# Performance work log

Measured on AMD Instinct MI355X. Metric: run time of the kernel, lower is better.

Reference implementation:

```python
import jax, jax.numpy as jnp
import numpy as np

NTOKENS = 50257
NHID = 1024
NPC = int(np.ceil(np.sqrt(NTOKENS)))            # 225 tokens per class
NCLASSES = int(np.ceil(NTOKENS / NPC))          # 224 classes
BATCH = 1024
INITRANGE = 0.1


def setup_inputs() -> dict:
    key = jax.random.key(0)
    k1, k2, k3, k4 = jax.random.split(key, 4)
    inputs = jax.random.normal(k1, (BATCH, NHID), dtype=jnp.float32)
    labels = jax.random.randint(k2, (BATCH,), 0, NTOKENS, dtype=jnp.int64)
    layer_top_W = jax.random.uniform(k3, (NHID, NCLASSES), minval=-INITRANGE, maxval=INITRANGE, dtype=jnp.float32)
    layer_top_b = jnp.zeros((NCLASSES,), dtype=jnp.float32)
    layer_bottom_W = jax.random.uniform(k4, (NCLASSES, NHID, NPC), minval=-INITRANGE, maxval=INITRANGE, dtype=jnp.float32)
    layer_bottom_b = jnp.zeros((NCLASSES, NPC), dtype=jnp.float32)
    return {
        "inputs": inputs,
        "labels": labels,
        "layer_top_W": layer_top_W,
        "layer_top_b": layer_top_b,
        "layer_bottom_W": layer_bottom_W,
        "layer_bottom_b": layer_bottom_b,
    }


def reference(inputs, labels, layer_top_W, layer_top_b, layer_bottom_W, layer_bottom_b):
    batch_size = inputs.shape[0]
    # decompose label into (class, within-class) position; old-torch `/` on Long == floor div
    pos_top = labels // NPC            # [B]
    pos_bottom = labels % NPC          # [B]

    # top-level class distribution: [B, nclasses]
    top_logits = inputs @ layer_top_W + layer_top_b
    top_probs = jax.nn.softmax(top_logits, axis=1)

    # gather per-sample class weight slices and do batched matvec:
    # layer_bottom_W[pos_top]: [B, nhid, npc]
    bottom_logits = jnp.einsum("bd,bdc->bc", inputs, layer_bottom_W[pos_top]) + layer_bottom_b[pos_top]
    bottom_probs = jax.nn.softmax(bottom_logits, axis=1)

    rows = jnp.arange(batch_size)
    target_probs = top_probs[rows, pos_top] * bottom_probs[rows, pos_bottom]  # [B]
    return target_probs
```

## Files before the change

### kernel.cpp

```cpp
#include <hip/hip_runtime.h>
#include <math.h>

#define NTOK 50257
#define NHID 1024
#define NPC  225
#define NCLS 224
#define BATCH 1024

#define WS_ORDER_OFS 16
#define WS_ITEMS_OFS 8192
#define WS_PTOP_OFS  16384
#define MAX_ITEMS    352

__global__ __launch_bounds__(256) void k0_group(const int* __restrict__ labels,
                                                int* __restrict__ ws)
{
    __shared__ int cnt[256];
    __shared__ int scan[256];
    __shared__ int iscan[256];
    __shared__ int cur[256];
    const int tid = threadIdx.x;

    cnt[tid] = 0;
    __syncthreads();
    for (int i = tid; i < BATCH; i += 256)
        atomicAdd(&cnt[labels[i] / NPC], 1);
    __syncthreads();

    const int myc = (tid < NCLS) ? cnt[tid] : 0;
    const int myi = (myc + 7) >> 3;
    scan[tid]  = myc;
    iscan[tid] = myi;
    __syncthreads();
    for (int off = 1; off < 256; off <<= 1) {
        int a = (tid >= off) ? scan[tid - off]  : 0;
        int b = (tid >= off) ? iscan[tid - off] : 0;
        __syncthreads();
        scan[tid]  += a;
        iscan[tid] += b;
        __syncthreads();
    }
    const int sbase = scan[tid]  - myc;
    const int ibase = iscan[tid] - myi;
    if (tid == 255) ws[0] = iscan[255];
    cur[tid] = sbase;

    int4* items = (int4*)((char*)ws + WS_ITEMS_OFS);
    if (tid < NCLS) {
        for (int t = 0; t < myi; ++t)
            items[ibase + t] = make_int4(tid, sbase + 8 * t, min(8, myc - 8 * t), 0);
    }
    __syncthreads();

    int* order = ws + WS_ORDER_OFS;
    for (int i = tid; i < BATCH; i += 256) {
        int c = labels[i] / NPC;
        int p = atomicAdd(&cur[c], 1);
        order[p] = i;
    }
}

template <int LD, int COLS>
__device__ __forceinline__ void block_matvec8_softmax(
    float* __restrict__ sm,
    const float* __restrict__ W,
    const float* __restrict__ bias,
    int wave, int lane,
    int nt,
    const int* __restrict__ s_ids,
    const int* __restrict__ labels,
    bool bottom,
    const float* __restrict__ ptop,
    float* __restrict__ outp)
{
    float acc[8][4];
#pragma unroll
    for (int j = 0; j < 8; ++j)
#pragma unroll
        for (int k = 0; k < 4; ++k) acc[j][k] = 0.f;

    const int c0 = lane, c1 = lane + 64, c2 = lane + 128, c3 = lane + 192;
    const bool m3 = (c3 < COLS);
    const int d0 = wave * 128;
    const float* Wr = W + (size_t)d0 * LD;

    float w0 = Wr[c0], w1 = Wr[c1], w2 = Wr[c2], w3 = m3 ? Wr[c3] : 0.f;
#pragma unroll 4
    for (int dd = 0; dd < 128; ++dd) {
        const float cw0 = w0, cw1 = w1, cw2 = w2, cw3 = w3;
        const float* nr = Wr + (size_t)min(dd + 1, 127) * LD;
        w0 = nr[c0]; w1 = nr[c1]; w2 = nr[c2]; w3 = m3 ? nr[c3] : 0.f;
        const float4 a = *(const float4*)&sm[(d0 + dd) * 12 + 0];
        const float4 b = *(const float4*)&sm[(d0 + dd) * 12 + 4];
        const float xi[8] = {a.x, a.y, a.z, a.w, b.x, b.y, b.z, b.w};
#pragma unroll
        for (int j = 0; j < 8; ++j) {
            acc[j][0] = fmaf(xi[j], cw0, acc[j][0]);
            acc[j][1] = fmaf(xi[j], cw1, acc[j][1]);
            acc[j][2] = fmaf(xi[j], cw2, acc[j][2]);
            acc[j][3] = fmaf(xi[j], cw3, acc[j][3]);
        }
    }
    __syncthreads();

    float* red = sm;
    if (wave >= 4) {
#pragma unroll
        for (int j = 0; j < 8; ++j)
#pragma unroll
            for (int k = 0; k < 4; ++k) {
                int c = lane + 64 * k;
                if (c < COLS) red[((wave - 4) * 8 + j) * 232 + c] = acc[j][k];
            }
    }
    __syncthreads();
    if (wave < 4) {
#pragma unroll
        for (int j = 0; j < 8; ++j)
#pragma unroll
            for (int k = 0; k < 4; ++k) {
                int c = lane + 64 * k;
                if (c < COLS)
                    red[(wave * 8 + j) * 232 + c] += acc[j][k];
            }
    }
    __syncthreads();

    const int j = wave;
    if (j < nt) {
        const int s = s_ids[j];
        float v[4];
#pragma unroll
        for (int k = 0; k < 4; ++k) {
            int c = lane + 64 * k;
            v[k] = (c < COLS)
                     ? (red[(0 * 8 + j) * 232 + c] + red[(1 * 8 + j) * 232 + c] +
                        red[(2 * 8 + j) * 232 + c] + red[(3 * 8 + j) * 232 + c] +
                        bias[c])
                     : -INFINITY;
        }
        float m = fmaxf(fmaxf(v[0], v[1]), fmaxf(v[2], v[3]));
        for (int o = 32; o > 0; o >>= 1) m = fmaxf(m, __shfl_xor(m, o));
        float e = expf(v[0] - m) + expf(v[1] - m) + expf(v[2] - m) + expf(v[3] - m);
        for (int o = 32; o > 0; o >>= 1) e += __shfl_xor(e, o);
        const int lab = labels[s];
        const int tgt = bottom ? (lab % NPC) : (lab / NPC);
        if (lane == (tgt & 63)) {
            float p = expf(v[tgt >> 6] - m) / e;
            outp[s] = bottom ? (ptop[s] * p) : p;
        }
    }
}

__global__ __launch_bounds__(512) void k1_top(const float* __restrict__ X,
                                              const int* __restrict__ labels,
                                              const float* __restrict__ Wt,
                                              const float* __restrict__ bt,
                                              float* __restrict__ ptop)
{
    __shared__ __align__(16) float smem[12288];
    const int tid  = threadIdx.x;
    const int wave = tid >> 6;
    const int lane = tid & 63;
    const int sbase = blockIdx.x * 8;

    for (int idx = tid; idx < 2048; idx += 512) {
        const int j  = idx >> 8;
        const int d4 = idx & 255;
        const float4 v = ((const float4*)&X[(size_t)(sbase + j) * NHID])[d4];
        smem[(4 * d4 + 0) * 12 + j] = v.x;
        smem[(4 * d4 + 1) * 12 + j] = v.y;
        smem[(4 * d4 + 2) * 12 + j] = v.z;
        smem[(4 * d4 + 3) * 12 + j] = v.w;
    }
    __syncthreads();

    int s_ids[8];
#pragma unroll
    for (int j = 0; j < 8; ++j) s_ids[j] = sbase + j;

    block_matvec8_softmax<NCLS, NCLS>(smem, Wt, bt, wave, lane, 8, s_ids,
                                      labels, false, nullptr, ptop);
}

__global__ __launch_bounds__(512) void k2_bottom(const float* __restrict__ X,
                                                 const int* __restrict__ labels,
                                                 const float* __restrict__ Wb,
                                                 const float* __restrict__ bb,
                                                 const int* __restrict__ ws,
                                                 const float* __restrict__ ptop,
                                                 float* __restrict__ out)
{
    __shared__ __align__(16) float smem[12288];
    const int nitems = ws[0];
    if ((int)blockIdx.x >= nitems) return;
    const int4 item = ((const int4*)((const char*)ws + WS_ITEMS_OFS))[blockIdx.x];
    const int cls = item.x, s0 = item.y, nt = item.z;
    const int* order = ws + WS_ORDER_OFS;

    const int tid  = threadIdx.x;
    const int wave = tid >> 6;
    const int lane = tid & 63;

    int s_ids[8];
#pragma unroll
    for (int j = 0; j < 8; ++j) s_ids[j] = (j < nt) ? order[s0 + j] : 0;

    for (int idx = tid; idx < 2048; idx += 512) {
        const int j  = idx >> 8;
        const int d4 = idx & 255;
        float4 v = make_float4(0.f, 0.f, 0.f, 0.f);
        if (j < nt) v = ((const float4*)&X[(size_t)s_ids[j] * NHID])[d4];
        smem[(4 * d4 + 0) * 12 + j] = v.x;
        smem[(4 * d4 + 1) * 12 + j] = v.y;
        smem[(4 * d4 + 2) * 12 + j] = v.z;
        smem[(4 * d4 + 3) * 12 + j] = v.w;
    }
    __syncthreads();

    const float* W = Wb + (size_t)cls * (NHID * NPC);
    block_matvec8_softmax<NPC, NPC>(smem, W, bb + cls * NPC, wave, lane, nt,
                                    s_ids, labels, true, ptop, out);
}

extern "C" void kernel_launch(void* const* d_in, const int* in_sizes, int n_in,
                              void* d_out, int out_size, void* d_ws, size_t ws_size,
                              hipStream_t stream)
{
    const float* X      = (const float*)d_in[0];
    const int*   labels = (const int*)  d_in[1];
    const float* Wt     = (const float*)d_in[2];
    const float* bt     = (const float*)d_in[3];
    const float* Wb     = (const float*)d_in[4];
    const float* bb     = (const float*)d_in[5];
    float* out = (float*)d_out;
    int*   ws  = (int*)d_ws;
    float* ptop = (float*)((char*)d_ws + WS_PTOP_OFS);

    hipLaunchKernelGGL(k0_group, dim3(1), dim3(256), 0, stream, labels, ws);
    hipLaunchKernelGGL(k1_top, dim3(BATCH / 8), dim3(512), 0, stream,
                       X, labels, Wt, bt, ptop);
    hipLaunchKernelGGL(k2_bottom, dim3(MAX_ITEMS), dim3(512), 0, stream,
                       X, labels, Wb, bb, ws, ptop, out);
}
```

Baseline: 330.4 us.

## Fold grouping into top kernel, deepen weight prefetch, use nontemporal bottom loads

The label-grouping kernel now runs as an extra block of the top-layer kernel, which removes one launch and lets the grouping overlap with the top matvec. The weight-row prefetch in the matvec loop grows from one row ahead to a four-deep ring buffer, so more global loads are in flight per wave. Loads of the bottom-layer weights use nontemporal hints, since each class slice is streamed and not reused. The deeper prefetch raises register pressure, and the extra grouping block makes the top kernel's grid uneven.

```diff
diff --git a/kernel.cpp b/kernel.cpp
--- a/kernel.cpp
+++ b/kernel.cpp
@@ -12,61 +12,60 @@
 #define WS_PTOP_OFS  16384
 #define MAX_ITEMS    352
 
-__global__ __launch_bounds__(256) void k0_group(const int* __restrict__ labels,
-                                                int* __restrict__ ws)
+__device__ __forceinline__ void group_samples(const int* __restrict__ labels,
+                                              int* __restrict__ ws, int tid)
 {
     __shared__ int cnt[256];
     __shared__ int scan[256];
     __shared__ int iscan[256];
     __shared__ int cur[256];
-    const int tid = threadIdx.x;
-
-    cnt[tid] = 0;
-    __syncthreads();
-    for (int i = tid; i < BATCH; i += 256)
+
+    if (tid < 256) cnt[tid] = 0;
+    __syncthreads();
+    for (int i = tid; i < BATCH; i += 512)
         atomicAdd(&cnt[labels[i] / NPC], 1);
     __syncthreads();
 
-    const int myc = (tid < NCLS) ? cnt[tid] : 0;
-    const int myi = (myc + 7) >> 3;
-    scan[tid]  = myc;
-    iscan[tid] = myi;
+    int myc = 0, myi = 0;
+    if (tid < 256) {
+        myc = (tid < NCLS) ? cnt[tid] : 0;
+        myi = (myc + 7) >> 3;
+        scan[tid]  = myc;
+        iscan[tid] = myi;
+    }
     __syncthreads();
     for (int off = 1; off < 256; off <<= 1) {
-        int a = (tid >= off) ? scan[tid - off]  : 0;
-        int b = (tid >= off) ? iscan[tid - off] : 0;
+        int a = 0, b = 0;
+        if (tid < 256 && tid >= off) { a = scan[tid - off]; b = iscan[tid - off]; }
         __syncthreads();
-        scan[tid]  += a;
-        iscan[tid] += b;
+        if (tid < 256) { scan[tid] += a; iscan[tid] += b; }
         __syncthreads();
     }
-    const int sbase = scan[tid]  - myc;
-    const int ibase = iscan[tid] - myi;
-    if (tid == 255) ws[0] = iscan[255];
-    cur[tid] = sbase;
-
-    int4* items = (int4*)((char*)ws + WS_ITEMS_OFS);
-    if (tid < NCLS) {
-        for (int t = 0; t < myi; ++t)
-            items[ibase + t] = make_int4(tid, sbase + 8 * t, min(8, myc - 8 * t), 0);
-    }
-    __syncthreads();
-
+    if (tid < 256) {
+        const int sbase = scan[tid]  - myc;
+        const int ibase = iscan[tid] - myi;
+        if (tid == 255) ws[0] = iscan[255];
+        cur[tid] = sbase;
+        int4* items = (int4*)((char*)ws + WS_ITEMS_OFS);
+        if (tid < NCLS)
+            for (int t = 0; t < myi; ++t)
+                items[ibase + t] = make_int4(tid, sbase + 8 * t, min(8, myc - 8 * t), 0);
+    }
+    __syncthreads();
     int* order = ws + WS_ORDER_OFS;
-    for (int i = tid; i < BATCH; i += 256) {
+    for (int i = tid; i < BATCH; i += 512) {
         int c = labels[i] / NPC;
         int p = atomicAdd(&cur[c], 1);
         order[p] = i;
     }
 }
 
-template <int LD, int COLS>
+template <int LD, int COLS, bool NT>
 __device__ __forceinline__ void block_matvec8_softmax(
     float* __restrict__ sm,
     const float* __restrict__ W,
     const float* __restrict__ bias,
-    int wave, int lane,
-    int nt,
+    int wave, int lane, int nt,
     const int* __restrict__ s_ids,
     const int* __restrict__ labels,
     bool bottom,
@@ -84,12 +83,28 @@
     const int d0 = wave * 128;
     const float* Wr = W + (size_t)d0 * LD;
 
-    float w0 = Wr[c0], w1 = Wr[c1], w2 = Wr[c2], w3 = m3 ? Wr[c3] : 0.f;
+    auto ldrow = [&](int r, float* o) {
+        const float* p = Wr + (size_t)r * LD;
+        if (NT) {
+            o[0] = __builtin_nontemporal_load(p + c0);
+            o[1] = __builtin_nontemporal_load(p + c1);
+            o[2] = __builtin_nontemporal_load(p + c2);
+            o[3] = m3 ? __builtin_nontemporal_load(p + c3) : 0.f;
+        } else {
+            o[0] = p[c0]; o[1] = p[c1]; o[2] = p[c2];
+            o[3] = m3 ? p[c3] : 0.f;
+        }
+    };
+
+    float wbuf[4][4];
+    ldrow(0, wbuf[0]); ldrow(1, wbuf[1]); ldrow(2, wbuf[2]); ldrow(3, wbuf[3]);
+
 #pragma unroll 4
     for (int dd = 0; dd < 128; ++dd) {
-        const float cw0 = w0, cw1 = w1, cw2 = w2, cw3 = w3;
-        const float* nr = Wr + (size_t)min(dd + 1, 127) * LD;
-        w0 = nr[c0]; w1 = nr[c1]; w2 = nr[c2]; w3 = m3 ? nr[c3] : 0.f;
+        const int slot = dd & 3;
+        const float cw0 = wbuf[slot][0], cw1 = wbuf[slot][1],
+                    cw2 = wbuf[slot][2], cw3 = wbuf[slot][3];
+        ldrow(min(dd + 4, 127), wbuf[slot]);
         const float4 a = *(const float4*)&sm[(d0 + dd) * 12 + 0];
         const float4 b = *(const float4*)&sm[(d0 + dd) * 12 + 4];
         const float xi[8] = {a.x, a.y, a.z, a.w, b.x, b.y, b.z, b.w};
@@ -120,8 +135,7 @@
 #pragma unroll
             for (int k = 0; k < 4; ++k) {
                 int c = lane + 64 * k;
-                if (c < COLS)
-                    red[(wave * 8 + j) * 232 + c] += acc[j][k];
+                if (c < COLS) red[(wave * 8 + j) * 232 + c] += acc[j][k];
             }
     }
     __syncthreads();
@@ -156,10 +170,17 @@
                                               const int* __restrict__ labels,
                                               const float* __restrict__ Wt,
                                               const float* __restrict__ bt,
-                                              float* __restrict__ ptop)
+                                              float* __restrict__ ptop,
+                                              int* __restrict__ ws)
 {
     __shared__ __align__(16) float smem[12288];
-    const int tid  = threadIdx.x;
+    const int tid = threadIdx.x;
+
+    if (blockIdx.x == BATCH / 8) {
+        group_samples(labels, ws, tid);
+        return;
+    }
+
     const int wave = tid >> 6;
     const int lane = tid & 63;
     const int sbase = blockIdx.x * 8;
@@ -179,8 +200,8 @@
 #pragma unroll
     for (int j = 0; j < 8; ++j) s_ids[j] = sbase + j;
 
-    block_matvec8_softmax<NCLS, NCLS>(smem, Wt, bt, wave, lane, 8, s_ids,
-                                      labels, false, nullptr, ptop);
+    block_matvec8_softmax<NCLS, NCLS, false>(smem, Wt, bt, wave, lane, 8, s_ids,
+                                             labels, false, nullptr, ptop);
 }
 
 __global__ __launch_bounds__(512) void k2_bottom(const float* __restrict__ X,
@@ -219,8 +240,8 @@
     __syncthreads();
 
     const float* W = Wb + (size_t)cls * (NHID * NPC);
-    block_matvec8_softmax<NPC, NPC>(smem, W, bb + cls * NPC, wave, lane, nt,
-                                    s_ids, labels, true, ptop, out);
+    block_matvec8_softmax<NPC, NPC, true>(smem, W, bb + cls * NPC, wave, lane,
+                                          nt, s_ids, labels, true, ptop, out);
 }
 
 extern "C" void kernel_launch(void* const* d_in, const int* in_sizes, int n_in,
@@ -237,9 +258,8 @@
     int*   ws  = (int*)d_ws;
     float* ptop = (float*)((char*)d_ws + WS_PTOP_OFS);
 
-    hipLaunchKernelGGL(k0_group, dim3(1), dim3(256), 0, stream, labels, ws);
-    hipLaunchKernelGGL(k1_top, dim3(BATCH / 8), dim3(512), 0, stream,
-                       X, labels, Wt, bt, ptop);
+    hipLaunchKernelGGL(k1_top, dim3(BATCH / 8 + 1), dim3(512), 0, stream,
+                       X, labels, Wt, bt, ptop, ws);
     hipLaunchKernelGGL(k2_bottom, dim3(MAX_ITEMS), dim3(512), 0, stream,
                        X, labels, Wb, bb, ws, ptop, out);
 }
```

Measured after the change: 309.4 us. 1.07x faster.
